# Kernel optimization log

Hardware: AMD Instinct MI355X
Metric: run time of the kernel (lower is better)

The kernel has to match this reference:

```python
import jax, jax.numpy as jnp
import numpy as np

N = 100000   # nodes
E = 1600000  # edges
D = 128      # in = hid = out feature dim
EPS = 1e-5


def gcn_conv(x, W, b, src, dst, w, n):
    # PyG GCNConv: h = x W; symmetric normalization with self-loops already in (src,dst,w)
    h = x @ W                                        # [N, D]
    deg = jax.ops.segment_sum(w, dst, num_segments=n)
    dinv = jnp.where(deg > 0, deg ** -0.5, 0.0)
    norm = dinv[src] * w * dinv[dst]                 # [E+N]
    out = jax.ops.segment_sum(h[src] * norm[:, None], dst, num_segments=n)
    return out + b


def batch_norm(x, gamma, beta):
    m = x.mean(axis=0)
    v = x.var(axis=0)  # biased, as PyTorch uses for normalization
    return gamma * (x - m) * jax.lax.rsqrt(v + EPS) + beta


def setup_inputs() -> dict:
    key = jax.random.key(0)
    ks = jax.random.split(key, 10)
    x = jax.random.normal(ks[0], (N, D), dtype=jnp.float32)
    edge_index = jax.random.randint(ks[1], (2, E), 0, N, dtype=jnp.int64)
    edge_weight = jax.random.uniform(ks[2], (E,), dtype=jnp.float32)
    s = 1.0 / np.sqrt(D)
    W1 = jax.random.uniform(ks[3], (D, D), jnp.float32, -s, s)
    b1 = jax.random.uniform(ks[4], (D,), jnp.float32, -s, s)
    W2 = jax.random.uniform(ks[5], (D, D), jnp.float32, -s, s)
    b2 = jax.random.uniform(ks[6], (D,), jnp.float32, -s, s)
    g1 = jnp.ones((D,), jnp.float32); beta1 = jnp.zeros((D,), jnp.float32)
    g2 = jnp.ones((D,), jnp.float32); beta2 = jnp.zeros((D,), jnp.float32)
    return {"x": x, "edge_index": edge_index, "edge_weight": edge_weight,
            "W1": W1, "b1": b1, "W2": W2, "b2": b2,
            "g1": g1, "beta1": beta1, "g2": g2, "beta2": beta2}


def reference(x, edge_index, edge_weight, W1, b1, W2, b2, g1, beta1, g2, beta2):
    loops = jnp.arange(N, dtype=edge_index.dtype)
    src = jnp.concatenate([edge_index[0], loops])
    dst = jnp.concatenate([edge_index[1], loops])
    w = jnp.concatenate([edge_weight, jnp.ones((N,), edge_weight.dtype)])
    # layer 1: GCNConv -> BN -> relu (dropout inactive in eval)
    h = gcn_conv(x, W1, b1, src, dst, w, N)
    h = jax.nn.relu(batch_norm(h, g1, beta1))
    # layer 2
    h = gcn_conv(h, W2, b2, src, dst, w, N)
    h = jax.nn.relu(batch_norm(h, g2, beta2))
    return h
```

## Files before the change

kernel.cpp:

```cpp
#include <hip/hip_runtime.h>
#include <hip/hip_bf16.h>

#define NN 100000
#define EE 1600000
#define DD 128
#define CAP 56
#define NB 391
#define CAPB 6144
#define NRG 6250
#define BN_EPS 1e-5f

typedef __attribute__((ext_vector_type(8))) short short8;
typedef __attribute__((ext_vector_type(4))) float f32x4;
typedef __attribute__((ext_vector_type(4))) unsigned int u32x4;

__device__ __forceinline__ float bfu2f(unsigned short u) {
    return __uint_as_float(((unsigned int)u) << 16);
}
__device__ __forceinline__ unsigned short f2bfu(float f) {
    unsigned int u = __float_as_uint(f);
    unsigned int r = (u + 0x7fffu + ((u >> 16) & 1u)) >> 16;
    return (unsigned short)r;
}
__device__ __forceinline__ void atomAddF(float* p, float v) {
    unsafeAtomicAdd(p, v);
}
__device__ __forceinline__ float ldF(const void* __restrict__ p, int isf32, size_t idx) {
    return isf32 ? ((const float*)p)[idx]
                 : bfu2f(((const unsigned short*)p)[idx]);
}
__device__ __forceinline__ int edge_at(const int* __restrict__ ei, int is64, unsigned int pos) {
    return is64 ? ei[(size_t)pos * 2] : ei[pos];
}

__global__ __launch_bounds__(256) void prep2(const int* __restrict__ ei,
                                             const unsigned int* __restrict__ g1w,
                                             const void* __restrict__ W1,
                                             const void* __restrict__ W2,
                                             int* __restrict__ flags,
                                             unsigned int* __restrict__ cursor,
                                             float* __restrict__ stats,
                                             unsigned short* __restrict__ Wt1,
                                             unsigned short* __restrict__ Wt2) {
    int t = threadIdx.x;
    int b = blockIdx.x;
    int isf32 = (g1w[0] == 0x3F800000u) ? 1 : 0;
    if (b == 0) {
        __shared__ int nz;
        if (t == 0) nz = 0;
        __syncthreads();
        if (ei[2 * t + 1] != 0) atomicExch(&nz, 1);
        __syncthreads();
        if (t == 0) {
            flags[0] = (nz == 0) ? 1 : 0;
            flags[1] = isf32;
        }
        stats[t] = 0.f;
        stats[512 + t] = 0.f;
    } else if (b == 129) {
        for (int i = t; i < 512; i += 256) cursor[i] = 0;
    } else {
        int i = (b - 1) * 256 + t;
        if (i < 16384) {
            int r = i >> 7, c = i & 127;
            Wt1[c * DD + r] = f2bfu(ldF(W1, isf32, i));
        } else {
            int j = i - 16384;
            int r = j >> 7, c = j & 127;
            Wt2[c * DD + r] = f2bfu(ldF(W2, isf32, j));
        }
    }
}

__device__ __forceinline__ void load_arow(const void* __restrict__ Xv, int isf32,
                                          int row, int quad, short8* dst) {
#pragma unroll
    for (int k4 = 0; k4 < 4; ++k4) {
        int k = k4 * 32 + quad * 8;
        if (isf32) {
            const float* xf = (const float*)Xv + (size_t)row * DD + k;
            float4 f0 = *(const float4*)xf;
            float4 f1 = *(const float4*)(xf + 4);
            short8 a;
            a[0] = (short)f2bfu(f0.x); a[1] = (short)f2bfu(f0.y);
            a[2] = (short)f2bfu(f0.z); a[3] = (short)f2bfu(f0.w);
            a[4] = (short)f2bfu(f1.x); a[5] = (short)f2bfu(f1.y);
            a[6] = (short)f2bfu(f1.z); a[7] = (short)f2bfu(f1.w);
            dst[k4] = a;
        } else {
            dst[k4] = *(const short8*)((const short*)Xv + (size_t)row * DD + k);
        }
    }
}

__global__ __launch_bounds__(256) void fatk(const void* __restrict__ Xv,
                                            const int* __restrict__ flags,
                                            const unsigned short* __restrict__ Wt,
                                            unsigned short* __restrict__ H,
                                            const int* __restrict__ ei,
                                            const void* __restrict__ w,
                                            uint2* __restrict__ staging,
                                            unsigned int* __restrict__ cursor) {
    unsigned int g = blockIdx.x;
    unsigned int q = g / 3u, r = g % 3u;
    if (r == 2u) {
        __shared__ unsigned int cnt[NB], base[NB];
        for (int i = threadIdx.x; i < NB; i += 256) cnt[i] = 0;
        __syncthreads();
        int is64 = flags[0], isf32 = flags[1];
        unsigned int e0 = q * 2048u;
        unsigned int lo[8], hi[8], rk[8];
        int bk[8];
#pragma unroll
        for (int i = 0; i < 8; ++i) {
            unsigned int e = e0 + i * 256u + threadIdx.x;
            bk[i] = -1;
            if (e < EE) {
                int s = edge_at(ei, is64, e);
                int d = edge_at(ei, is64, EE + e);
                float wv = ldF(w, isf32, e);
                unsigned int wfix = __float2uint_rn(wv * 16777216.0f);
                wfix = wfix > 0xFFFFFFu ? 0xFFFFFFu : wfix;
                lo[i] = ((unsigned int)f2bfu(wv) << 17) | (unsigned int)s;
                hi[i] = (wfix << 8) | (unsigned int)(d & 255);
                bk[i] = d >> 8;
                rk[i] = atomicAdd(&cnt[bk[i]], 1u);
            }
        }
        __syncthreads();
        for (int i = threadIdx.x; i < NB; i += 256)
            base[i] = cnt[i] ? atomicAdd(&cursor[i], cnt[i]) : 0u;
        __syncthreads();
#pragma unroll
        for (int i = 0; i < 8; ++i) {
            if (bk[i] >= 0) {
                unsigned int pos = base[bk[i]] + rk[i];
                if (pos < CAPB)
                    staging[(size_t)bk[i] * CAPB + pos] = make_uint2(lo[i], hi[i]);
            }
        }
    } else {
        int gid = (int)(q * 2u + r);
        int isf32 = flags[1];
        int lane = threadIdx.x & 63;
        int wave = threadIdx.x >> 6;
        int m = lane & 15, quad = lane >> 4;
        int n0 = wave * 32;
        const short* Ws = (const short*)Wt;
        short8 B0[4], B1[4];
#pragma unroll
        for (int k4 = 0; k4 < 4; ++k4) {
            int k = k4 * 32 + quad * 8;
            B0[k4] = *(const short8*)(Ws + (size_t)(n0 + m) * DD + k);
            B1[k4] = *(const short8*)(Ws + (size_t)(n0 + 16 + m) * DD + k);
        }
        int rgbase = gid * 4;
        short8 aC[4], aN[4];
        int rg0 = min(rgbase, NRG - 1);
        load_arow(Xv, isf32, rg0 * 16 + m, quad, aC);
#pragma unroll
        for (int rg = 0; rg < 4; ++rg) {
            int rgg = min(rgbase + rg, NRG - 1);
            if (rg < 3) {
                int rgn = min(rgbase + rg + 1, NRG - 1);
                load_arow(Xv, isf32, rgn * 16 + m, quad, aN);
            }
            f32x4 acc0 = {0.f, 0.f, 0.f, 0.f};
            f32x4 acc1 = {0.f, 0.f, 0.f, 0.f};
#pragma unroll
            for (int k4 = 0; k4 < 4; ++k4) {
                acc0 = __builtin_amdgcn_mfma_f32_16x16x32_bf16(aC[k4], B0[k4], acc0, 0, 0, 0);
                acc1 = __builtin_amdgcn_mfma_f32_16x16x32_bf16(aC[k4], B1[k4], acc1, 0, 0, 0);
            }
            int row0 = rgg * 16;
#pragma unroll
            for (int rr = 0; rr < 4; ++rr) {
                int crow = quad * 4 + rr;
                H[(size_t)(row0 + crow) * DD + n0 + m]      = f2bfu(acc0[rr]);
                H[(size_t)(row0 + crow) * DD + n0 + 16 + m] = f2bfu(acc1[rr]);
            }
#pragma unroll
            for (int k4 = 0; k4 < 4; ++k4) aC[k4] = aN[k4];
        }
    }
}

__global__ __launch_bounds__(256) void ellbuild(const uint2* __restrict__ staging,
                                                const unsigned int* __restrict__ cursor,
                                                unsigned int* __restrict__ ell,
                                                unsigned long long* __restrict__ meta) {
    __shared__ __align__(16) unsigned int lrow[256 * CAP];
    __shared__ unsigned int lcnt[256], lws[256];
    int b = blockIdx.x, t = threadIdx.x;
    lcnt[t] = 0; lws[t] = 0;
    {
        uint4 z = make_uint4(0, 0, 0, 0);
        uint4* lp = (uint4*)lrow;
        for (int j = t; j < 256 * CAP / 4; j += 256) lp[j] = z;
    }
    __syncthreads();
    unsigned int rc = cursor[b];
    if (rc > CAPB) rc = CAPB;
    const uint2* S = staging + (size_t)b * CAPB;
    for (unsigned int j = t; j < rc; j += 256) {
        uint2 rec = S[j];
        unsigned int dl = rec.y & 255u;
        unsigned int rk = atomicAdd(&lcnt[dl], 1u);
        atomicAdd(&lws[dl], rec.y >> 8);
        if (rk < CAP) lrow[dl * CAP + rk] = rec.x;
    }
    __syncthreads();
    int nrows = NN - b * 256;
    if (nrows > 256) nrows = 256;
    int nv = nrows * (CAP / 4);
    uint4* dst = (uint4*)(ell + (size_t)b * 256 * CAP);
    const uint4* src = (const uint4*)lrow;
    for (int j = t; j < nv; j += 256) dst[j] = src[j];
    if (t < nrows) {
        unsigned int c = lcnt[t];
        unsigned int c8 = (c + 7u) & ~7u;
        if (c8 > CAP) c8 = CAP;
        float dv = rsqrtf(1.0f + (float)lws[t] * (1.0f / 16777216.0f));
        meta[b * 256 + t] = ((unsigned long long)c8 << 32) |
                            (unsigned long long)__float_as_uint(dv);
    }
}

__global__ __launch_bounds__(256) void gather_agg(const unsigned short* __restrict__ H,
                                                  const unsigned long long* __restrict__ meta,
                                                  const unsigned int* __restrict__ ell,
                                                  unsigned short* __restrict__ A) {
    int wave = threadIdx.x >> 6;
    int lane = threadIdx.x & 63;
    int half = lane >> 5;
    int sub = lane & 31;
    int n = blockIdx.x * 4 + wave;
    unsigned long long m = meta[n];
    int cnt8 = (int)(m >> 32);
    if (cnt8 > CAP) cnt8 = CAP;
    float di = __uint_as_float((unsigned int)m);
    const unsigned short* Hf = H + sub * 4;
    const float* dvp = (const float*)meta;
    float a0 = 0.f, a1 = 0.f, a2 = 0.f, a3 = 0.f;
    if (half == 0) {
        ushort4 hs = *(const ushort4*)(Hf + ((size_t)n << 7));
        a0 = bfu2f(hs.x) * di; a1 = bfu2f(hs.y) * di;
        a2 = bfu2f(hs.z) * di; a3 = bfu2f(hs.w) * di;
    }
    const unsigned int* row = ell + (size_t)n * CAP + (half << 2);
    for (int i = 0; i < cnt8; i += 8) {
        u32x4 qv = __builtin_nontemporal_load((const u32x4*)(row + i));
        unsigned int qa[4] = {qv.x, qv.y, qv.z, qv.w};
#pragma unroll
        for (int t = 0; t < 4; ++t) {
            unsigned int ent = qa[t];
            int s = (int)(ent & 0x1FFFFu);
            float wv = __uint_as_float((ent >> 1) & 0xFFFF0000u);
            float we = wv * dvp[2 * s];
            ushort4 h = *(const ushort4*)(Hf + ((size_t)s << 7));
            a0 = fmaf(bfu2f(h.x), we, a0);
            a1 = fmaf(bfu2f(h.y), we, a1);
            a2 = fmaf(bfu2f(h.z), we, a2);
            a3 = fmaf(bfu2f(h.w), we, a3);
        }
    }
    a0 += __shfl_down(a0, 32);
    a1 += __shfl_down(a1, 32);
    a2 += __shfl_down(a2, 32);
    a3 += __shfl_down(a3, 32);
    if (half == 0) {
        ushort4 o;
        o.x = f2bfu(a0 * di);
        o.y = f2bfu(a1 * di);
        o.z = f2bfu(a2 * di);
        o.w = f2bfu(a3 * di);
        *(ushort4*)(A + ((size_t)n << 7) + sub * 4) = o;
    }
}

__global__ __launch_bounds__(256) void gemm2(const unsigned short* __restrict__ A,
                                             const float* __restrict__ scale,
                                             const float* __restrict__ shift,
                                             const unsigned short* __restrict__ Wt,
                                             unsigned short* __restrict__ H) {
    __shared__ __align__(16) float lsc[DD], lsh[DD];
    if (threadIdx.x < DD) {
        lsc[threadIdx.x] = scale[threadIdx.x];
        lsh[threadIdx.x] = shift[threadIdx.x];
    }
    __syncthreads();
    int lane = threadIdx.x & 63;
    int wave = threadIdx.x >> 6;
    int m = lane & 15, quad = lane >> 4;
    int n0 = wave * 32;
    const short* Ws = (const short*)Wt;
    short8 B0[4], B1[4];
#pragma unroll
    for (int k4 = 0; k4 < 4; ++k4) {
        int k = k4 * 32 + quad * 8;
        B0[k4] = *(const short8*)(Ws + (size_t)(n0 + m) * DD + k);
        B1[k4] = *(const short8*)(Ws + (size_t)(n0 + 16 + m) * DD + k);
    }
    int rgbase = blockIdx.x * 4;
    short8 aC[4], aN[4];
#define LOADA2(dst, RG)                                                           \
    {                                                                             \
        int rr_ = (RG) * 16 + m;                                                  \
        const short* ap_ = (const short*)A + (size_t)rr_ * DD;                    \
        _Pragma("unroll")                                                         \
        for (int k4_ = 0; k4_ < 4; ++k4_) {                                       \
            int k_ = k4_ * 32 + quad * 8;                                         \
            short8 raw_ = *(const short8*)(ap_ + k_);                             \
            float4 sc0_ = *(const float4*)(lsc + k_);                             \
            float4 sc1_ = *(const float4*)(lsc + k_ + 4);                         \
            float4 sh0_ = *(const float4*)(lsh + k_);                             \
            float4 sh1_ = *(const float4*)(lsh + k_ + 4);                         \
            short8 a_;                                                            \
            a_[0] = (short)f2bfu(fmaxf(fmaf(bfu2f((unsigned short)raw_[0]), sc0_.x, sh0_.x), 0.f)); \
            a_[1] = (short)f2bfu(fmaxf(fmaf(bfu2f((unsigned short)raw_[1]), sc0_.y, sh0_.y), 0.f)); \
            a_[2] = (short)f2bfu(fmaxf(fmaf(bfu2f((unsigned short)raw_[2]), sc0_.z, sh0_.z), 0.f)); \
            a_[3] = (short)f2bfu(fmaxf(fmaf(bfu2f((unsigned short)raw_[3]), sc0_.w, sh0_.w), 0.f)); \
            a_[4] = (short)f2bfu(fmaxf(fmaf(bfu2f((unsigned short)raw_[4]), sc1_.x, sh1_.x), 0.f)); \
            a_[5] = (short)f2bfu(fmaxf(fmaf(bfu2f((unsigned short)raw_[5]), sc1_.y, sh1_.y), 0.f)); \
            a_[6] = (short)f2bfu(fmaxf(fmaf(bfu2f((unsigned short)raw_[6]), sc1_.z, sh1_.z), 0.f)); \
            a_[7] = (short)f2bfu(fmaxf(fmaf(bfu2f((unsigned short)raw_[7]), sc1_.w, sh1_.w), 0.f)); \
            dst[k4_] = a_;                                                        \
        }                                                                         \
    }
    int rg0 = min(rgbase, NRG - 1);
    LOADA2(aC, rg0);
#pragma unroll
    for (int rg = 0; rg < 4; ++rg) {
        int rgg = min(rgbase + rg, NRG - 1);
        if (rg < 3) {
            int rgn = min(rgbase + rg + 1, NRG - 1);
            LOADA2(aN, rgn);
        }
        f32x4 acc0 = {0.f, 0.f, 0.f, 0.f};
        f32x4 acc1 = {0.f, 0.f, 0.f, 0.f};
#pragma unroll
        for (int k4 = 0; k4 < 4; ++k4) {
            acc0 = __builtin_amdgcn_mfma_f32_16x16x32_bf16(aC[k4], B0[k4], acc0, 0, 0, 0);
            acc1 = __builtin_amdgcn_mfma_f32_16x16x32_bf16(aC[k4], B1[k4], acc1, 0, 0, 0);
        }
        int row0 = rgg * 16;
#pragma unroll
        for (int rr = 0; rr < 4; ++rr) {
            int crow = quad * 4 + rr;
            H[(size_t)(row0 + crow) * DD + n0 + m]      = f2bfu(acc0[rr]);
            H[(size_t)(row0 + crow) * DD + n0 + 16 + m] = f2bfu(acc1[rr]);
        }
#pragma unroll
        for (int k4 = 0; k4 < 4; ++k4) aC[k4] = aN[k4];
    }
#undef LOADA2
}

__global__ __launch_bounds__(256) void bn_stats(const unsigned short* __restrict__ A,
                                                float* __restrict__ gsum,
                                                float* __restrict__ gss) {
    __shared__ float ls[8][128], lq[8][128];
    int t = threadIdx.x;
    int fq = t & 31;
    int rsub = t >> 5;
    float s0 = 0.f, s1 = 0.f, s2 = 0.f, s3 = 0.f;
    float q0 = 0.f, q1 = 0.f, q2 = 0.f, q3 = 0.f;
    for (int r = blockIdx.x * 8 + rsub; r < NN; r += gridDim.x * 8) {
        ushort4 v = *(const ushort4*)(A + (size_t)r * DD + fq * 4);
        float x0 = bfu2f(v.x), x1 = bfu2f(v.y), x2 = bfu2f(v.z), x3 = bfu2f(v.w);
        s0 += x0; s1 += x1; s2 += x2; s3 += x3;
        q0 += x0 * x0; q1 += x1 * x1; q2 += x2 * x2; q3 += x3 * x3;
    }
    ls[rsub][fq * 4 + 0] = s0; ls[rsub][fq * 4 + 1] = s1;
    ls[rsub][fq * 4 + 2] = s2; ls[rsub][fq * 4 + 3] = s3;
    lq[rsub][fq * 4 + 0] = q0; lq[rsub][fq * 4 + 1] = q1;
    lq[rsub][fq * 4 + 2] = q2; lq[rsub][fq * 4 + 3] = q3;
    __syncthreads();
    if (t < 128) {
        float a = 0.f, b = 0.f;
#pragma unroll
        for (int r = 0; r < 8; ++r) { a += ls[r][t]; b += lq[r][t]; }
        atomAddF(&gsum[t], a);
        atomAddF(&gss[t], b);
    }
}

__global__ __launch_bounds__(128) void bn_final(const float* __restrict__ gsum,
                                                const float* __restrict__ gss,
                                                const void* __restrict__ gamma,
                                                const void* __restrict__ beta,
                                                const int* __restrict__ flags,
                                                float* __restrict__ scale,
                                                float* __restrict__ shift) {
    int f = threadIdx.x;
    int isf32 = flags[1];
    float m = gsum[f] * (1.0f / NN);
    float v = gss[f] * (1.0f / NN) - m * m;
    v = fmaxf(v, 0.0f);
    float sc = ldF(gamma, isf32, f) * rsqrtf(v + BN_EPS);
    scale[f] = sc;
    shift[f] = ldF(beta, isf32, f) - m * sc;
}

__global__ __launch_bounds__(256) void bn_apply(const unsigned short* __restrict__ A,
                                                const float* __restrict__ scale,
                                                const float* __restrict__ shift,
                                                const int* __restrict__ flags,
                                                void* __restrict__ out) {
    int i = blockIdx.x * 256 + threadIdx.x;
    int f = (i & 31) * 4;
    ushort4 v4 = ((const ushort4*)A)[i];
    float r0 = fmaxf(fmaf(bfu2f(v4.x), scale[f + 0], shift[f + 0]), 0.f);
    float r1 = fmaxf(fmaf(bfu2f(v4.y), scale[f + 1], shift[f + 1]), 0.f);
    float r2 = fmaxf(fmaf(bfu2f(v4.z), scale[f + 2], shift[f + 2]), 0.f);
    float r3 = fmaxf(fmaf(bfu2f(v4.w), scale[f + 3], shift[f + 3]), 0.f);
    if (flags[1]) {
        ((float4*)out)[i] = make_float4(r0, r1, r2, r3);
    } else {
        ushort4 o;
        o.x = f2bfu(r0); o.y = f2bfu(r1); o.z = f2bfu(r2); o.w = f2bfu(r3);
        ((ushort4*)out)[i] = o;
    }
}

extern "C" void kernel_launch(void* const* d_in, const int* in_sizes, int n_in,
                              void* d_out, int out_size, void* d_ws, size_t ws_size,
                              hipStream_t stream) {
    const void* x   = d_in[0];
    const int*  ei  = (const int*)d_in[1];
    const void* ew  = d_in[2];
    const void* W1  = d_in[3];
    const void* W2  = d_in[5];
    const void* g1  = d_in[7];
    const void* be1 = d_in[8];
    const void* g2  = d_in[9];
    const void* be2 = d_in[10];

    char* ws = (char*)d_ws;
    float* stats         = (float*)ws;
    int*   flags         = (int*)(ws + 4096);
    unsigned short* Wt1  = (unsigned short*)(ws + 4224);
    unsigned short* Wt2  = (unsigned short*)(ws + 36992);
    unsigned long long* meta = (unsigned long long*)(ws + 69760);
    unsigned int* ell    = (unsigned int*)(ws + 869760);
    unsigned short* Hbuf = (unsigned short*)(ws + 23269760);
    unsigned short* A    = (unsigned short*)(ws + 48869760);
    uint2* staging       = (uint2*)(ws + 48869760);
    unsigned int* cursor = (unsigned int*)(ws + 48869760 + 19218432);
    float* gsum1 = stats,       *gss1 = stats + 128, *scale1 = stats + 256, *shift1 = stats + 384;
    float* gsum2 = stats + 512, *gss2 = stats + 640, *scale2 = stats + 768, *shift2 = stats + 896;

    prep2<<<130, 256, 0, stream>>>(ei, (const unsigned int*)g1, W1, W2,
                                   flags, cursor, stats, Wt1, Wt2);

    fatk<<<2346, 256, 0, stream>>>(x, flags, Wt1, Hbuf, ei, ew, staging, cursor);
    ellbuild<<<NB, 256, 0, stream>>>(staging, cursor, ell, meta);
    gather_agg<<<25000, 256, 0, stream>>>(Hbuf, meta, ell, A);
    bn_stats<<<512, 256, 0, stream>>>(A, gsum1, gss1);
    bn_final<<<1, 128, 0, stream>>>(gsum1, gss1, g1, be1, flags, scale1, shift1);

    gemm2<<<1563, 256, 0, stream>>>(A, scale1, shift1, Wt2, Hbuf);
    gather_agg<<<25000, 256, 0, stream>>>(Hbuf, meta, ell, A);
    bn_stats<<<512, 256, 0, stream>>>(A, gsum2, gss2);
    bn_final<<<1, 128, 0, stream>>>(gsum2, gss2, g2, be2, flags, scale2, shift2);
    bn_apply<<<12500, 256, 0, stream>>>(A, scale2, shift2, flags, d_out);
}
```

Baseline: 403.3 us.

## Fuse BatchNorm statistics into gather aggregation epilogue with spread atomics

Drops the separate bn_stats kernels. Each gather_agg block now reduces per-feature sum and sum of squares of its four rows in LDS and atomically adds them into one of 16 spread accumulator copies. bn_final sums those copies. The accumulators reuse the Wt1 workspace region and are zeroed inside ellbuild. The edge loop is also unrolled to handle 16 entries per iteration. This removes two full re-reads of the aggregated activations and two launches, at the cost of a block-wide sync and many global float atomics in every gather block.

```diff
diff --git a/kernel.cpp b/kernel.cpp
--- a/kernel.cpp
+++ b/kernel.cpp
@@ -8,6 +8,7 @@
 #define NB 391
 #define CAPB 6144
 #define NRG 6250
+#define NC 16
 #define BN_EPS 1e-5f
 
 typedef __attribute__((ext_vector_type(8))) short short8;
@@ -188,10 +189,12 @@
 __global__ __launch_bounds__(256) void ellbuild(const uint2* __restrict__ staging,
                                                 const unsigned int* __restrict__ cursor,
                                                 unsigned int* __restrict__ ell,
-                                                unsigned long long* __restrict__ meta) {
+                                                unsigned long long* __restrict__ meta,
+                                                float* __restrict__ gacc) {
     __shared__ __align__(16) unsigned int lrow[256 * CAP];
     __shared__ unsigned int lcnt[256], lws[256];
     int b = blockIdx.x, t = threadIdx.x;
+    if (b < 32) gacc[b * 256 + t] = 0.f;
     lcnt[t] = 0; lws[t] = 0;
     {
         uint4 z = make_uint4(0, 0, 0, 0);
@@ -226,10 +229,29 @@
     }
 }
 
+__device__ __forceinline__ void proc4(u32x4 qv, const float* __restrict__ dvp,
+                                      const unsigned short* __restrict__ Hf,
+                                      float& a0, float& a1, float& a2, float& a3) {
+    unsigned int qa[4] = {qv.x, qv.y, qv.z, qv.w};
+#pragma unroll
+    for (int t = 0; t < 4; ++t) {
+        unsigned int ent = qa[t];
+        int s = (int)(ent & 0x1FFFFu);
+        float we = __uint_as_float((ent >> 1) & 0xFFFF0000u) * dvp[2 * s];
+        ushort4 h = *(const ushort4*)(Hf + ((size_t)s << 7));
+        a0 = fmaf(bfu2f(h.x), we, a0);
+        a1 = fmaf(bfu2f(h.y), we, a1);
+        a2 = fmaf(bfu2f(h.z), we, a2);
+        a3 = fmaf(bfu2f(h.w), we, a3);
+    }
+}
+
 __global__ __launch_bounds__(256) void gather_agg(const unsigned short* __restrict__ H,
                                                   const unsigned long long* __restrict__ meta,
                                                   const unsigned int* __restrict__ ell,
-                                                  unsigned short* __restrict__ A) {
+                                                  unsigned short* __restrict__ A,
+                                                  float* __restrict__ gacc) {
+    __shared__ float lsum[4][128], lss[4][128];
     int wave = threadIdx.x >> 6;
     int lane = threadIdx.x & 63;
     int half = lane >> 5;
@@ -237,7 +259,6 @@
     int n = blockIdx.x * 4 + wave;
     unsigned long long m = meta[n];
     int cnt8 = (int)(m >> 32);
-    if (cnt8 > CAP) cnt8 = CAP;
     float di = __uint_as_float((unsigned int)m);
     const unsigned short* Hf = H + sub * 4;
     const float* dvp = (const float*)meta;
@@ -248,21 +269,17 @@
         a2 = bfu2f(hs.z) * di; a3 = bfu2f(hs.w) * di;
     }
     const unsigned int* row = ell + (size_t)n * CAP + (half << 2);
-    for (int i = 0; i < cnt8; i += 8) {
-        u32x4 qv = __builtin_nontemporal_load((const u32x4*)(row + i));
-        unsigned int qa[4] = {qv.x, qv.y, qv.z, qv.w};
-#pragma unroll
-        for (int t = 0; t < 4; ++t) {
-            unsigned int ent = qa[t];
-            int s = (int)(ent & 0x1FFFFu);
-            float wv = __uint_as_float((ent >> 1) & 0xFFFF0000u);
-            float we = wv * dvp[2 * s];
-            ushort4 h = *(const ushort4*)(Hf + ((size_t)s << 7));
-            a0 = fmaf(bfu2f(h.x), we, a0);
-            a1 = fmaf(bfu2f(h.y), we, a1);
-            a2 = fmaf(bfu2f(h.z), we, a2);
-            a3 = fmaf(bfu2f(h.w), we, a3);
-        }
+    int i16 = cnt8 & ~15;
+    int i = 0;
+    for (; i < i16; i += 16) {
+        u32x4 q0 = __builtin_nontemporal_load((const u32x4*)(row + i));
+        u32x4 q1 = __builtin_nontemporal_load((const u32x4*)(row + i + 8));
+        proc4(q0, dvp, Hf, a0, a1, a2, a3);
+        proc4(q1, dvp, Hf, a0, a1, a2, a3);
+    }
+    if (i < cnt8) {
+        u32x4 q0 = __builtin_nontemporal_load((const u32x4*)(row + i));
+        proc4(q0, dvp, Hf, a0, a1, a2, a3);
     }
     a0 += __shfl_down(a0, 32);
     a1 += __shfl_down(a1, 32);
@@ -275,6 +292,21 @@
         o.z = f2bfu(a2 * di);
         o.w = f2bfu(a3 * di);
         *(ushort4*)(A + ((size_t)n << 7) + sub * 4) = o;
+        float v0 = bfu2f(o.x), v1 = bfu2f(o.y), v2 = bfu2f(o.z), v3 = bfu2f(o.w);
+        int fb = sub * 4;
+        lsum[wave][fb + 0] = v0; lsum[wave][fb + 1] = v1;
+        lsum[wave][fb + 2] = v2; lsum[wave][fb + 3] = v3;
+        lss[wave][fb + 0] = v0 * v0; lss[wave][fb + 1] = v1 * v1;
+        lss[wave][fb + 2] = v2 * v2; lss[wave][fb + 3] = v3 * v3;
+    }
+    __syncthreads();
+    int t = threadIdx.x;
+    if (t < 128) {
+        float s = lsum[0][t] + lsum[1][t] + lsum[2][t] + lsum[3][t];
+        float q = lss[0][t] + lss[1][t] + lss[2][t] + lss[3][t];
+        float* gb = gacc + (blockIdx.x & (NC - 1)) * 256;
+        atomAddF(&gb[t], s);
+        atomAddF(&gb[128 + t], q);
     }
 }
 
@@ -356,37 +388,7 @@
 #undef LOADA2
 }
 
-__global__ __launch_bounds__(256) void bn_stats(const unsigned short* __restrict__ A,
-                                                float* __restrict__ gsum,
-                                                float* __restrict__ gss) {
-    __shared__ float ls[8][128], lq[8][128];
-    int t = threadIdx.x;
-    int fq = t & 31;
-    int rsub = t >> 5;
-    float s0 = 0.f, s1 = 0.f, s2 = 0.f, s3 = 0.f;
-    float q0 = 0.f, q1 = 0.f, q2 = 0.f, q3 = 0.f;
-    for (int r = blockIdx.x * 8 + rsub; r < NN; r += gridDim.x * 8) {
-        ushort4 v = *(const ushort4*)(A + (size_t)r * DD + fq * 4);
-        float x0 = bfu2f(v.x), x1 = bfu2f(v.y), x2 = bfu2f(v.z), x3 = bfu2f(v.w);
-        s0 += x0; s1 += x1; s2 += x2; s3 += x3;
-        q0 += x0 * x0; q1 += x1 * x1; q2 += x2 * x2; q3 += x3 * x3;
-    }
-    ls[rsub][fq * 4 + 0] = s0; ls[rsub][fq * 4 + 1] = s1;
-    ls[rsub][fq * 4 + 2] = s2; ls[rsub][fq * 4 + 3] = s3;
-    lq[rsub][fq * 4 + 0] = q0; lq[rsub][fq * 4 + 1] = q1;
-    lq[rsub][fq * 4 + 2] = q2; lq[rsub][fq * 4 + 3] = q3;
-    __syncthreads();
-    if (t < 128) {
-        float a = 0.f, b = 0.f;
-#pragma unroll
-        for (int r = 0; r < 8; ++r) { a += ls[r][t]; b += lq[r][t]; }
-        atomAddF(&gsum[t], a);
-        atomAddF(&gss[t], b);
-    }
-}
-
-__global__ __launch_bounds__(128) void bn_final(const float* __restrict__ gsum,
-                                                const float* __restrict__ gss,
+__global__ __launch_bounds__(128) void bn_final(const float* __restrict__ gacc,
                                                 const void* __restrict__ gamma,
                                                 const void* __restrict__ beta,
                                                 const int* __restrict__ flags,
@@ -394,8 +396,14 @@
                                                 float* __restrict__ shift) {
     int f = threadIdx.x;
     int isf32 = flags[1];
-    float m = gsum[f] * (1.0f / NN);
-    float v = gss[f] * (1.0f / NN) - m * m;
+    float s = 0.f, ss = 0.f;
+#pragma unroll
+    for (int c = 0; c < NC; ++c) {
+        s  += gacc[c * 256 + f];
+        ss += gacc[c * 256 + 128 + f];
+    }
+    float m = s * (1.0f / NN);
+    float v = ss * (1.0f / NN) - m * m;
     v = fmaxf(v, 0.0f);
     float sc = ldF(gamma, isf32, f) * rsqrtf(v + BN_EPS);
     scale[f] = sc;
@@ -447,21 +455,21 @@
     unsigned short* A    = (unsigned short*)(ws + 48869760);
     uint2* staging       = (uint2*)(ws + 48869760);
     unsigned int* cursor = (unsigned int*)(ws + 48869760 + 19218432);
-    float* gsum1 = stats,       *gss1 = stats + 128, *scale1 = stats + 256, *shift1 = stats + 384;
-    float* gsum2 = stats + 512, *gss2 = stats + 640, *scale2 = stats + 768, *shift2 = stats + 896;
+    float* gaccL1 = (float*)(ws + 4224);
+    float* gaccL2 = (float*)(ws + 4224 + 16384);
+    float* scale1 = stats + 256, *shift1 = stats + 384;
+    float* scale2 = stats + 768, *shift2 = stats + 896;
 
     prep2<<<130, 256, 0, stream>>>(ei, (const unsigned int*)g1, W1, W2,
                                    flags, cursor, stats, Wt1, Wt2);
 
     fatk<<<2346, 256, 0, stream>>>(x, flags, Wt1, Hbuf, ei, ew, staging, cursor);
-    ellbuild<<<NB, 256, 0, stream>>>(staging, cursor, ell, meta);
-    gather_agg<<<25000, 256, 0, stream>>>(Hbuf, meta, ell, A);
-    bn_stats<<<512, 256, 0, stream>>>(A, gsum1, gss1);
-    bn_final<<<1, 128, 0, stream>>>(gsum1, gss1, g1, be1, flags, scale1, shift1);
+    ellbuild<<<NB, 256, 0, stream>>>(staging, cursor, ell, meta, gaccL1);
+    gather_agg<<<25000, 256, 0, stream>>>(Hbuf, meta, ell, A, gaccL1);
+    bn_final<<<1, 128, 0, stream>>>(gaccL1, g1, be1, flags, scale1, shift1);
 
     gemm2<<<1563, 256, 0, stream>>>(A, scale1, shift1, Wt2, Hbuf);
-    gather_agg<<<25000, 256, 0, stream>>>(Hbuf, meta, ell, A);
-    bn_stats<<<512, 256, 0, stream>>>(A, gsum2, gss2);
-    bn_final<<<1, 128, 0, stream>>>(gsum2, gss2, g2, be2, flags, scale2, shift2);
+    gather_agg<<<25000, 256, 0, stream>>>(Hbuf, meta, ell, A, gaccL2);
+    bn_final<<<1, 128, 0, stream>>>(gaccL2, g2, be2, flags, scale2, shift2);
     bn_apply<<<12500, 256, 0, stream>>>(A, scale2, shift2, flags, d_out);
 }
```

Measured after the change: 372.4 us. 7.7% less time.
